# Performance work log

Hardware: AMD Instinct MI355X
Metric: run time of the kernel (lower is better)

Reference implementation:

```python
import jax, jax.numpy as jnp
import numpy as np
import math

B, S, D, H, HD, DC, FF, E, K = 4, 2048, 576, 9, 64, 64, 1536, 8, 2
EPS = 1e-6


def _rms(x):
    # RMSNorm with weight=ones (module instantiates a fresh RMSNorm in forward)
    return x / jnp.sqrt(jnp.mean(x * x, axis=-1, keepdims=True) + EPS)


def _expert(h, wa, wb, wc):
    return (jax.nn.gelu(h @ wa, approximate=False) * (h @ wc)) @ wb


def _forward(x, q_w, kv_w, o_w, gate_w, w1, w2, w3, sw1, sw2, sw3):
    # ---------------- MLA ----------------
    xn = _rms(x)
    q = (xn @ q_w).reshape(B, S, H, HD)
    kv = (xn @ kv_w).reshape(B, S, H, 2 * DC)
    k, v = kv[..., :DC], kv[..., DC:]
    # RoPE (complex-pair form) applied to q only, as in the source
    theta = 1.0 / (10000.0 ** (jnp.arange(0, HD, 2, dtype=jnp.float32) / HD))
    freqs = jnp.arange(S, dtype=jnp.float32)[:, None] * theta[None, :]  # [S, HD/2]
    cos = jnp.cos(freqs)[None, :, None, :]
    sin = jnp.sin(freqs)[None, :, None, :]
    qp = q.reshape(B, S, H, HD // 2, 2)
    qe, qo = qp[..., 0], qp[..., 1]
    q = jnp.stack([qe * cos - qo * sin, qe * sin + qo * cos], axis=-1).reshape(B, S, H, HD)
    # NOTE: source matmul attends head-vs-head per token: [B,S,H,HD] x [B,S,DC,H] -> [B,S,H,H]
    attn = jnp.einsum('bshd,bstd->bsht', q, k) / math.sqrt(HD)
    attn = jax.nn.softmax(attn, axis=-1)
    ao = jnp.einsum('bsht,bstd->bshd', attn, v)  # [B,S,H,DC]
    # faithful to torch: transpose(1,2).contiguous().view(B,S,D)
    ao = ao.transpose(0, 2, 1, 3).reshape(B, S, D)
    x = ao @ o_w + x
    # ---------------- MoE ----------------
    xn = _rms(x)
    gw = jax.nn.softmax(xn @ gate_w, axis=-1)  # [B,S,E]
    tw, ti = jax.lax.top_k(gw, K)
    tw = tw / jnp.sum(tw, axis=-1, keepdims=True)
    # combine weights per expert: zero for unselected experts (same math as masked loop)
    comb = jnp.sum(tw[..., None] * jax.nn.one_hot(ti, E, dtype=x.dtype), axis=-2)  # [B,S,E]
    h1 = jax.nn.gelu(jnp.einsum('bsd,edf->ebsf', xn, w1), approximate=False)
    h3 = jnp.einsum('bsd,edf->ebsf', xn, w3)
    eo = jnp.einsum('ebsf,efd->ebsd', h1 * h3, w2)  # [E,B,S,D]
    moe_out = jnp.einsum('ebsd,bse->bsd', eo, comb)
    shared = _expert(xn, sw1, sw2, sw3)
    return moe_out + shared + x


def setup_inputs() -> dict:
    key = jax.random.key(0)
    ks = jax.random.split(key, 11)
    s = 0.02
    return {
        'x': jax.random.normal(ks[0], (B, S, D), dtype=jnp.float32),
        'q_w': jax.random.normal(ks[1], (D, D), dtype=jnp.float32) * s,
        'kv_w': jax.random.normal(ks[2], (D, H * 2 * DC), dtype=jnp.float32) * s,
        'o_w': jax.random.normal(ks[3], (D, D), dtype=jnp.float32) * s,
        'gate_w': jax.random.normal(ks[4], (D, E), dtype=jnp.float32) * s,
        'w1': jax.random.normal(ks[5], (E, D, FF), dtype=jnp.float32) * s,
        'w2': jax.random.normal(ks[6], (E, FF, D), dtype=jnp.float32) * s,
        'w3': jax.random.normal(ks[7], (E, D, FF), dtype=jnp.float32) * s,
        'sw1': jax.random.normal(ks[8], (D, FF), dtype=jnp.float32) * s,
        'sw2': jax.random.normal(ks[9], (FF, D), dtype=jnp.float32) * s,
        'sw3': jax.random.normal(ks[10], (D, FF), dtype=jnp.float32) * s,
    }


def reference(x, q_w, kv_w, o_w, gate_w, w1, w2, w3, sw1, sw2, sw3):
    return _forward(x, q_w, kv_w, o_w, gate_w, w1, w2, w3, sw1, sw2, sw3)
```

## Files before the change

### kernel.cpp

```cpp
#include <hip/hip_runtime.h>
#include <math.h>

#define B_  4
#define S_  2048
#define D_  576
#define H_  9
#define HD_ 64
#define FF_ 1536
#define E_  8
#define TOK (B_*S_)
#define T1ROWS 17408

typedef unsigned int   u32x4  __attribute__((ext_vector_type(4)));
typedef unsigned short u16x8  __attribute__((ext_vector_type(8)));
typedef __bf16         bf16x8 __attribute__((ext_vector_type(8)));
typedef _Float16       f16x8  __attribute__((ext_vector_type(8)));
typedef float          f32x4  __attribute__((ext_vector_type(4)));

__device__ __forceinline__ float b2f(unsigned short u) {
    union { unsigned int i; float f; } v; v.i = ((unsigned int)u) << 16; return v.f;
}
__device__ __forceinline__ unsigned short f2b(float f) {
    unsigned int u = __builtin_bit_cast(unsigned int, f);
    unsigned int r = 0x7fffu + ((u >> 16) & 1u);
    return (unsigned short)((u + r) >> 16);
}

__global__ __launch_bounds__(256)
void rmsnorm_k(const float* __restrict__ x, unsigned short* __restrict__ xn) {
    int tok = blockIdx.x, tid = threadIdx.x;
    const float* xr = x + (size_t)tok * D_;
    float v0 = xr[tid];
    float v1 = xr[tid + 256];
    float v2 = (tid < D_ - 512) ? xr[tid + 512] : 0.f;
    float ss = v0*v0 + v1*v1 + v2*v2;
    #pragma unroll
    for (int d = 1; d < 64; d <<= 1) ss += __shfl_xor(ss, d, 64);
    __shared__ float red[4];
    if ((tid & 63) == 0) red[tid >> 6] = ss;
    __syncthreads();
    float tot = red[0] + red[1] + red[2] + red[3];
    float rms = rsqrtf(tot / (float)D_ + 1e-6f);
    unsigned short* orow = xn + (size_t)tok * D_;
    orow[tid]       = f2b(v0 * rms);
    orow[tid + 256] = f2b(v1 * rms);
    if (tid < D_ - 512) orow[tid + 512] = f2b(v2 * rms);
}

__global__ __launch_bounds__(256)
void rms32_k(const float* __restrict__ x, float* __restrict__ xn) {
    int tok = blockIdx.x, tid = threadIdx.x;
    const float* xr = x + (size_t)tok * D_;
    float v0 = xr[tid];
    float v1 = xr[tid + 256];
    float v2 = (tid < D_ - 512) ? xr[tid + 512] : 0.f;
    float ss = v0*v0 + v1*v1 + v2*v2;
    #pragma unroll
    for (int d = 1; d < 64; d <<= 1) ss += __shfl_xor(ss, d, 64);
    __shared__ float red[4];
    if ((tid & 63) == 0) red[tid >> 6] = ss;
    __syncthreads();
    float tot = red[0] + red[1] + red[2] + red[3];
    float rms = rsqrtf(tot / (float)D_ + 1e-6f);
    float* orow = xn + (size_t)tok * D_;
    orow[tid]       = v0 * rms;
    orow[tid + 256] = v1 * rms;
    if (tid < D_ - 512) orow[tid + 512] = v2 * rms;
}

__global__ __launch_bounds__(256)
void convw_k(const float* __restrict__ src, unsigned short* __restrict__ dst,
             int K, int N, long long sstr, long long dstr)
{
    __shared__ unsigned short t[64][72];
    int n0 = blockIdx.x * 64, k0 = blockIdx.y * 64;
    const float* s = src + (long long)blockIdx.z * sstr;
    unsigned short* d = dst + (long long)blockIdx.z * dstr;
    int tx = threadIdx.x & 63, ty = threadIdx.x >> 6;
    #pragma unroll
    for (int i = 0; i < 16; ++i) {
        int k = i * 4 + ty;
        t[k][tx] = f2b(s[(size_t)(k0 + k) * N + n0 + tx]);
    }
    __syncthreads();
    int r = threadIdx.x >> 3, c8 = (threadIdx.x & 7) * 8;
    #pragma unroll
    for (int it = 0; it < 2; ++it, r += 32) {
        u16x8 v;
        #pragma unroll
        for (int j = 0; j < 8; ++j) v[j] = t[c8 + j][r];
        *(u16x8*)&d[(size_t)(n0 + r) * K + k0 + c8] = v;
    }
}

template<int BN, int EPI>
__global__ __launch_bounds__(256)
void gemmS_k(const float* __restrict__ A, const float* __restrict__ Bm,
             float* __restrict__ Cout, const float* __restrict__ resid,
             int M, int N, int K, int ldb)
{
    constexpr int BM = 128, BK = 64, LDT = BK + 8;
    constexpr int WM = BM / 2, WN = BN / 2, MI = WM / 16, NJ = WN / 16;
    __shared__ alignas(16) _Float16 Ah[BM][LDT], Al[BM][LDT];
    __shared__ alignas(16) _Float16 Bh[BN][LDT], Bl[BN][LDT];
    const int tid  = threadIdx.x;
    const int bn0  = blockIdx.x * BN, bm0 = blockIdx.y * BM;
    const int lane = tid & 63, wave = tid >> 6;
    const int l    = lane & 15, quad = lane >> 4;
    const int wm   = wave >> 1, wn = wave & 1;

    f32x4 accH[MI][NJ], accL[MI][NJ];
    #pragma unroll
    for (int mi = 0; mi < MI; ++mi)
        #pragma unroll
        for (int nj = 0; nj < NJ; ++nj) {
            accH[mi][nj] = (f32x4){0.f, 0.f, 0.f, 0.f};
            accL[mi][nj] = (f32x4){0.f, 0.f, 0.f, 0.f};
        }

    const int nK = K / BK;
    for (int kc = 0; kc < nK; ++kc) {
        __syncthreads();
        #pragma unroll
        for (int i = 0; i < (BM * BK) / 2048; ++i) {
            int u = i * 256 + tid;
            int r = u >> 3, c8 = (u & 7) * 8;
            const float* ga = A + (size_t)(bm0 + r) * K + kc * BK + c8;
            f16x8 hh, ll;
            #pragma unroll
            for (int j = 0; j < 8; ++j) {
                float v = ga[j];
                _Float16 h = (_Float16)v;
                hh[j] = h;
                ll[j] = (_Float16)((v - (float)h) * 2048.0f);
            }
            *(f16x8*)&Ah[r][c8] = hh;
            *(f16x8*)&Al[r][c8] = ll;
        }
        #pragma unroll
        for (int i = 0; i < (BN * BK) / 2048; ++i) {
            int u = i * 256 + tid;
            int n = u % BN, k8 = (u / BN) * 8;
            const float* gB = Bm + (size_t)(kc * BK + k8) * ldb + bn0 + n;
            f16x8 hh, ll;
            #pragma unroll
            for (int j = 0; j < 8; ++j) {
                float v = gB[(size_t)j * ldb];
                _Float16 h = (_Float16)v;
                hh[j] = h;
                ll[j] = (_Float16)((v - (float)h) * 2048.0f);
            }
            *(f16x8*)&Bh[n][k8] = hh;
            *(f16x8*)&Bl[n][k8] = ll;
        }
        __syncthreads();
        #pragma unroll
        for (int ks = 0; ks < BK; ks += 32) {
            f16x8 ah[MI], al[MI], bh[NJ], bl[NJ];
            #pragma unroll
            for (int mi = 0; mi < MI; ++mi) {
                ah[mi] = *(const f16x8*)&Ah[wm * WM + mi * 16 + l][ks + quad * 8];
                al[mi] = *(const f16x8*)&Al[wm * WM + mi * 16 + l][ks + quad * 8];
            }
            #pragma unroll
            for (int nj = 0; nj < NJ; ++nj) {
                bh[nj] = *(const f16x8*)&Bh[wn * WN + nj * 16 + l][ks + quad * 8];
                bl[nj] = *(const f16x8*)&Bl[wn * WN + nj * 16 + l][ks + quad * 8];
            }
            #pragma unroll
            for (int mi = 0; mi < MI; ++mi)
                #pragma unroll
                for (int nj = 0; nj < NJ; ++nj) {
                    accH[mi][nj] = __builtin_amdgcn_mfma_f32_16x16x32_f16(
                        ah[mi], bh[nj], accH[mi][nj], 0, 0, 0);
                    accL[mi][nj] = __builtin_amdgcn_mfma_f32_16x16x32_f16(
                        ah[mi], bl[nj], accL[mi][nj], 0, 0, 0);
                    accL[mi][nj] = __builtin_amdgcn_mfma_f32_16x16x32_f16(
                        al[mi], bh[nj], accL[mi][nj], 0, 0, 0);
                }
        }
    }
    #pragma unroll
    for (int mi = 0; mi < MI; ++mi)
        #pragma unroll
        for (int nj = 0; nj < NJ; ++nj)
            #pragma unroll
            for (int r = 0; r < 4; ++r) {
                int row = bm0 + wm * WM + mi * 16 + quad * 4 + r;
                int col = bn0 + wn * WN + nj * 16 + l;
                float v = accH[mi][nj][r] + accL[mi][nj][r] * (1.0f / 2048.0f);
                size_t idx = (size_t)row * N + col;
                if constexpr (EPI == 0) Cout[idx] = v;
                else                    Cout[idx] = v + resid[idx];
            }
}

template<int ROUTED>
__global__ __launch_bounds__(256, 2)
void gemm13_k(const unsigned short* __restrict__ A,
              const unsigned short* __restrict__ B1,
              const unsigned short* __restrict__ B3,
              unsigned short* __restrict__ T1o,
              const int* __restrict__ eidx,
              const int* __restrict__ counts,
              const int* __restrict__ offs,
              int M, int N, long long bstr)
{
    constexpr int BM = 128, BN = 128, BK = 64, LDT = BK + 8;
    constexpr int MI = 4, NJ = 4;
    __shared__ alignas(16) unsigned short As[BM][LDT];
    __shared__ alignas(16) unsigned short Bs1[BN][LDT];
    __shared__ alignas(16) unsigned short Bs3[BN][LDT];
    __shared__ int rowbuf[BM];
    const int tid  = threadIdx.x;
    const int bn0  = blockIdx.x * BN, bm0 = blockIdx.y * BM;
    const int lane = tid & 63, wave = tid >> 6;
    const int l    = lane & 15, quad = lane >> 4;
    const int wm   = wave >> 1, wn = wave & 1;
    const int rs   = tid >> 3, c8 = (tid & 7) * 8;

    int cnt = M, crow0 = 0;
    if constexpr (ROUTED) {
        int e = blockIdx.z;
        cnt = counts[e];
        if (bm0 >= cnt) return;
        crow0 = offs[e];
        B1 += (long long)e * bstr;
        B3 += (long long)e * bstr;
        if (tid < BM) {
            int rr = bm0 + tid;
            rowbuf[tid] = (rr < cnt) ? eidx[e * TOK + rr] : 0;
        }
        __syncthreads();
    }

    f32x4 acc1[MI][NJ], acc3[MI][NJ];
    #pragma unroll
    for (int mi = 0; mi < MI; ++mi)
        #pragma unroll
        for (int nj = 0; nj < NJ; ++nj) {
            acc1[mi][nj] = (f32x4){0.f, 0.f, 0.f, 0.f};
            acc3[mi][nj] = (f32x4){0.f, 0.f, 0.f, 0.f};
        }

    const int nK = D_ / BK;
    u32x4 ra[4], rb1[4], rb3[4];
    #pragma unroll
    for (int i = 0; i < 4; ++i) {
        int r = i * 32 + rs;
        int arow = ROUTED ? rowbuf[r] : (bm0 + r);
        ra[i]  = *(const u32x4*)(A  + (size_t)arow * D_ + c8);
        rb1[i] = *(const u32x4*)(B1 + (size_t)(bn0 + r) * D_ + c8);
        rb3[i] = *(const u32x4*)(B3 + (size_t)(bn0 + r) * D_ + c8);
    }
    for (int kc = 0; kc < nK; ++kc) {
        __syncthreads();
        #pragma unroll
        for (int i = 0; i < 4; ++i) {
            int r = i * 32 + rs;
            *(u32x4*)&As[r][c8]  = ra[i];
            *(u32x4*)&Bs1[r][c8] = rb1[i];
            *(u32x4*)&Bs3[r][c8] = rb3[i];
        }
        __syncthreads();
        if (kc + 1 < nK) {
            int ko = (kc + 1) * BK;
            #pragma unroll
            for (int i = 0; i < 4; ++i) {
                int r = i * 32 + rs;
                int arow = ROUTED ? rowbuf[r] : (bm0 + r);
                ra[i]  = *(const u32x4*)(A  + (size_t)arow * D_ + ko + c8);
                rb1[i] = *(const u32x4*)(B1 + (size_t)(bn0 + r) * D_ + ko + c8);
                rb3[i] = *(const u32x4*)(B3 + (size_t)(bn0 + r) * D_ + ko + c8);
            }
        }
        #pragma unroll
        for (int ks = 0; ks < BK; ks += 32) {
            bf16x8 af[MI], b1f[NJ], b3f[NJ];
            #pragma unroll
            for (int mi = 0; mi < MI; ++mi)
                af[mi] = __builtin_bit_cast(bf16x8,
                    *(const u32x4*)&As[wm * 64 + mi * 16 + l][ks + quad * 8]);
            #pragma unroll
            for (int nj = 0; nj < NJ; ++nj) {
                b1f[nj] = __builtin_bit_cast(bf16x8,
                    *(const u32x4*)&Bs1[wn * 64 + nj * 16 + l][ks + quad * 8]);
                b3f[nj] = __builtin_bit_cast(bf16x8,
                    *(const u32x4*)&Bs3[wn * 64 + nj * 16 + l][ks + quad * 8]);
            }
            #pragma unroll
            for (int mi = 0; mi < MI; ++mi)
                #pragma unroll
                for (int nj = 0; nj < NJ; ++nj) {
                    acc1[mi][nj] = __builtin_amdgcn_mfma_f32_16x16x32_bf16(
                        af[mi], b1f[nj], acc1[mi][nj], 0, 0, 0);
                    acc3[mi][nj] = __builtin_amdgcn_mfma_f32_16x16x32_bf16(
                        af[mi], b3f[nj], acc3[mi][nj], 0, 0, 0);
                }
        }
    }
    #pragma unroll
    for (int mi = 0; mi < MI; ++mi)
        #pragma unroll
        for (int nj = 0; nj < NJ; ++nj)
            #pragma unroll
            for (int r = 0; r < 4; ++r) {
                int lrow = bm0 + wm * 64 + mi * 16 + quad * 4 + r;
                int col  = bn0 + wn * 64 + nj * 16 + l;
                float hv = b2f(f2b(acc1[mi][nj][r]));
                float g  = 0.5f * hv * (1.0f + erff(hv * 0.70710678118654752f));
                T1o[(size_t)(crow0 + lrow) * N + col] = f2b(g * acc3[mi][nj][r]);
            }
}

template<int BN, int EPI, int ROUTED, int WB>
__global__ __launch_bounds__(256)
void gemm_k(const unsigned short* __restrict__ A,
            const void* __restrict__ Bm,
            void* __restrict__ Cout,
            const void* __restrict__ resid,
            const float* __restrict__ wgt,
            const int* __restrict__ eidx,
            const int* __restrict__ counts,
            const int* __restrict__ offs,
            int M, int N, int K, int ldb, long long bstr)
{
    constexpr int BM = 128, BK = 64, LDT = BK + 8;
    constexpr int WM = BM / 2, WN = BN / 2, MI = WM / 16, NJ = WN / 16;
    constexpr int AIT = (BM * BK) / 2048, BIT = (BN * BK) / 2048;
    __shared__ alignas(16) unsigned short As[BM][LDT];
    __shared__ alignas(16) unsigned short Bs[BN][LDT];
    __shared__ int rowbuf[BM];
    const int tid  = threadIdx.x;
    const int bn0  = blockIdx.x * BN, bm0 = blockIdx.y * BM;
    const int lane = tid & 63, wave = tid >> 6;
    const int l    = lane & 15, quad = lane >> 4;
    const int wm   = wave >> 1, wn = wave & 1;

    int cnt = M, crow0 = 0, ebase = 0;
    long long boff = 0;
    if constexpr (ROUTED) {
        int e = blockIdx.z;
        cnt = counts[e];
        if (bm0 >= cnt) return;
        crow0 = offs[e];
        ebase = e * TOK;
        boff  = (long long)e * bstr;
        if (tid < BM) {
            int rr = bm0 + tid;
            rowbuf[tid] = (rr < cnt) ? eidx[ebase + rr] : 0;
        }
        __syncthreads();
    }

    f32x4 acc[MI][NJ];
    #pragma unroll
    for (int mi = 0; mi < MI; ++mi)
        #pragma unroll
        for (int nj = 0; nj < NJ; ++nj) acc[mi][nj] = (f32x4){0.f, 0.f, 0.f, 0.f};

    const int nK = K / BK;
    u32x4 pa[AIT], pb[BIT];
    if constexpr (WB == 1) {
        const unsigned short* Bt = (const unsigned short*)Bm + boff;
        #pragma unroll
        for (int i = 0; i < AIT; ++i) {
            int r = i * 32 + (tid >> 3), c8 = (tid & 7) * 8;
            int arow;
            if constexpr (ROUTED && EPI != 5) arow = rowbuf[r];
            else if constexpr (ROUTED)        arow = crow0 + bm0 + r;
            else                              arow = bm0 + r;
            pa[i] = *(const u32x4*)(A + (size_t)arow * K + c8);
        }
        #pragma unroll
        for (int i = 0; i < BIT; ++i) {
            int n = i * 32 + (tid >> 3), c8 = (tid & 7) * 8;
            pb[i] = *(const u32x4*)(Bt + (size_t)(bn0 + n) * ldb + c8);
        }
    }
    for (int kc = 0; kc < nK; ++kc) {
        __syncthreads();
        if constexpr (WB == 1) {
            #pragma unroll
            for (int i = 0; i < AIT; ++i) {
                int r = i * 32 + (tid >> 3), c8 = (tid & 7) * 8;
                *(u32x4*)&As[r][c8] = pa[i];
            }
            #pragma unroll
            for (int i = 0; i < BIT; ++i) {
                int n = i * 32 + (tid >> 3), c8 = (tid & 7) * 8;
                *(u32x4*)&Bs[n][c8] = pb[i];
            }
        } else {
            #pragma unroll
            for (int i = 0; i < AIT; ++i) {
                int u = i * 256 + tid;
                int r = u >> 3, c8 = (u & 7) * 8;
                int arow;
                if constexpr (ROUTED && EPI != 5) arow = rowbuf[r];
                else if constexpr (ROUTED)        arow = crow0 + bm0 + r;
                else                              arow = bm0 + r;
                *(u32x4*)&As[r][c8] =
                    *(const u32x4*)(A + (size_t)arow * K + kc * BK + c8);
            }
            const float* Bf = (const float*)Bm + boff;
            #pragma unroll
            for (int i = 0; i < BIT; ++i) {
                int u = i * 256 + tid;
                int n = u % BN, k8 = (u / BN) * 8;
                const float* gB = Bf + (size_t)(kc * BK + k8) * ldb + bn0 + n;
                u16x8 tmp;
                #pragma unroll
                for (int j = 0; j < 8; ++j) tmp[j] = f2b(gB[(size_t)j * ldb]);
                *(u16x8*)&Bs[n][k8] = tmp;
            }
        }
        __syncthreads();
        if constexpr (WB == 1) {
            if (kc + 1 < nK) {
                int ko = (kc + 1) * BK;
                const unsigned short* Bt = (const unsigned short*)Bm + boff;
                #pragma unroll
                for (int i = 0; i < AIT; ++i) {
                    int r = i * 32 + (tid >> 3), c8 = (tid & 7) * 8;
                    int arow;
                    if constexpr (ROUTED && EPI != 5) arow = rowbuf[r];
                    else if constexpr (ROUTED)        arow = crow0 + bm0 + r;
                    else                              arow = bm0 + r;
                    pa[i] = *(const u32x4*)(A + (size_t)arow * K + ko + c8);
                }
                #pragma unroll
                for (int i = 0; i < BIT; ++i) {
                    int n = i * 32 + (tid >> 3), c8 = (tid & 7) * 8;
                    pb[i] = *(const u32x4*)(Bt + (size_t)(bn0 + n) * ldb + ko + c8);
                }
            }
        }
        #pragma unroll
        for (int ks = 0; ks < BK; ks += 32) {
            bf16x8 af[MI], bfr[NJ];
            #pragma unroll
            for (int mi = 0; mi < MI; ++mi)
                af[mi] = __builtin_bit_cast(bf16x8,
                    *(const u32x4*)&As[wm * WM + mi * 16 + l][ks + quad * 8]);
            #pragma unroll
            for (int nj = 0; nj < NJ; ++nj)
                bfr[nj] = __builtin_bit_cast(bf16x8,
                    *(const u32x4*)&Bs[wn * WN + nj * 16 + l][ks + quad * 8]);
            #pragma unroll
            for (int mi = 0; mi < MI; ++mi)
                #pragma unroll
                for (int nj = 0; nj < NJ; ++nj)
                    acc[mi][nj] = __builtin_amdgcn_mfma_f32_16x16x32_bf16(
                        af[mi], bfr[nj], acc[mi][nj], 0, 0, 0);
        }
    }
    #pragma unroll
    for (int mi = 0; mi < MI; ++mi)
        #pragma unroll
        for (int nj = 0; nj < NJ; ++nj)
            #pragma unroll
            for (int r = 0; r < 4; ++r) {
                int lrow = bm0 + wm * WM + mi * 16 + quad * 4 + r;
                int col  = bn0 + wn * WN + nj * 16 + l;
                float v = acc[mi][nj][r];
                if constexpr (EPI == 0) {
                    ((unsigned short*)Cout)[(size_t)(crow0 + lrow) * N + col] = f2b(v);
                } else if constexpr (EPI == 3) {
                    size_t ix = (size_t)(crow0 + lrow) * N + col;
                    float hv = b2f(((const unsigned short*)resid)[ix]);
                    float g = 0.5f * hv * (1.0f + erff(hv * 0.70710678118654752f));
                    ((unsigned short*)Cout)[ix] = f2b(g * v);
                } else if constexpr (EPI == 4) {
                    ((float*)Cout)[(size_t)lrow * N + col] += v;
                } else {
                    if (lrow < cnt) {
                        int   tok = rowbuf[lrow - bm0];
                        float sc  = wgt[ebase + lrow];
                        atomicAdd(&((float*)Cout)[(size_t)tok * N + col], sc * v);
                    }
                }
            }
}

__global__ __launch_bounds__(256)
void attn32_k(const float* __restrict__ q,
              const float* __restrict__ kv,
              float* __restrict__ ao,
              int pos0)
{
    int pl   = blockIdx.x * 4 + (threadIdx.x >> 6);
    int lane = threadIdx.x & 63;
    int pos  = pos0 + pl;
    int b = pos >> 11, s = pos & 2047;

    const float* qp  = q  + (size_t)pl * 576;
    const float* kvp = kv + (size_t)pl * 1152;

    int i = lane >> 1;
    float theta = powf(10000.f, -(float)i * (1.0f / 32.0f));
    float sn, cs;
    sincosf((float)s * theta, &sn, &cs);

    float qr[H_], kr[H_], vr[H_];
    #pragma unroll
    for (int h = 0; h < H_; ++h) {
        float qv = qp[h * 64 + lane];
        float qo = __shfl_xor(qv, 1, 64);
        qr[h] = (lane & 1) ? (qo * sn + qv * cs) : (qv * cs - qo * sn);
        kr[h] = kvp[h * 128 + lane];
        vr[h] = kvp[h * 128 + 64 + lane];
    }

    #pragma unroll
    for (int h = 0; h < H_; ++h) {
        float sc[H_];
        #pragma unroll
        for (int t = 0; t < H_; ++t) {
            float p = qr[h] * kr[t];
            #pragma unroll
            for (int d = 1; d < 64; d <<= 1) p += __shfl_xor(p, d, 64);
            sc[t] = p * 0.125f;
        }
        float mx = sc[0];
        #pragma unroll
        for (int t = 1; t < H_; ++t) mx = fmaxf(mx, sc[t]);
        float ssum = 0.f;
        #pragma unroll
        for (int t = 0; t < H_; ++t) { sc[t] = __expf(sc[t] - mx); ssum += sc[t]; }
        float inv = 1.0f / ssum;
        float ov = 0.f;
        #pragma unroll
        for (int t = 0; t < H_; ++t) ov += sc[t] * vr[t];
        ao[((size_t)(b * H_ + h) * S_ + s) * 64 + lane] = ov * inv;
    }
}

__global__ __launch_bounds__(256)
void gate1_k(const float* __restrict__ x2,
             const float* __restrict__ gw,
             float* __restrict__ tw,
             int*   __restrict__ tsel)
{
    int tok  = blockIdx.x * 4 + (threadIdx.x >> 6);
    int lane = threadIdx.x & 63;
    float acc[8];
    #pragma unroll
    for (int e = 0; e < 8; ++e) acc[e] = 0.f;
    float ss = 0.f;
    for (int d = lane; d < D_; d += 64) {
        float xv = x2[(size_t)tok * D_ + d];
        ss += xv * xv;
        const float* wr = gw + (size_t)d * 8;
        #pragma unroll
        for (int e = 0; e < 8; ++e) acc[e] += xv * wr[e];
    }
    #pragma unroll
    for (int d = 1; d < 64; d <<= 1) ss += __shfl_xor(ss, d, 64);
    #pragma unroll
    for (int e = 0; e < 8; ++e)
        #pragma unroll
        for (int d = 1; d < 64; d <<= 1) acc[e] += __shfl_xor(acc[e], d, 64);
    if (lane == 0) {
        float rms = rsqrtf(ss / (float)D_ + 1e-6f);
        #pragma unroll
        for (int e = 0; e < 8; ++e) acc[e] *= rms;
        float mx = acc[0];
        #pragma unroll
        for (int e = 1; e < 8; ++e) mx = fmaxf(mx, acc[e]);
        float g[8], ssum = 0.f;
        #pragma unroll
        for (int e = 0; e < 8; ++e) { g[e] = __expf(acc[e] - mx); ssum += g[e]; }
        #pragma unroll
        for (int e = 0; e < 8; ++e) g[e] /= ssum;
        int i1 = 0;
        #pragma unroll
        for (int e = 1; e < 8; ++e) if (g[e] > g[i1]) i1 = e;
        int i2 = -1;
        #pragma unroll
        for (int e = 0; e < 8; ++e)
            if (e != i1 && (i2 < 0 || g[e] > g[i2])) i2 = e;
        float s2 = g[i1] + g[i2];
        tw[(size_t)tok * 2 + 0] = g[i1] / s2;
        tw[(size_t)tok * 2 + 1] = g[i2] / s2;
        tsel[tok] = i1 | (i2 << 8);
    }
}

__global__ __launch_bounds__(256)
void gate2_k(const int*   __restrict__ tsel,
             const float* __restrict__ tw,
             float* __restrict__ wgt,
             int*   __restrict__ eidx,
             int*   __restrict__ counts)
{
    int e    = blockIdx.x;
    int tid  = threadIdx.x;
    int lane = tid & 63, wv = tid >> 6;
    __shared__ int wtot[4];
    int base = 0;
    for (int t0 = 0; t0 < TOK; t0 += 256) {
        int tok = t0 + tid;
        int s = tsel[tok];
        int hit = 0; float w = 0.f;
        if ((s & 255) == e)      { hit = 1; w = tw[(size_t)tok * 2 + 0]; }
        else if ((s >> 8) == e)  { hit = 1; w = tw[(size_t)tok * 2 + 1]; }
        unsigned long long m = __ballot(hit);
        int pre = __popcll(m & ((1ull << lane) - 1ull));
        if (lane == 0) wtot[wv] = __popcll(m);
        __syncthreads();
        int off = base;
        for (int q = 0; q < wv; ++q) off += wtot[q];
        if (hit) {
            int p = off + pre;
            eidx[e * TOK + p] = tok;
            wgt [e * TOK + p] = w;
        }
        base += wtot[0] + wtot[1] + wtot[2] + wtot[3];
        __syncthreads();
    }
    if (tid == 0) counts[e] = base;
}

__global__ void offs_k(const int* __restrict__ counts, int* __restrict__ offs) {
    if (threadIdx.x == 0) {
        int run = 0;
        for (int e = 0; e < 8; ++e) {
            offs[e] = run;
            run += ((counts[e] + 127) >> 7) << 7;
        }
    }
}

extern "C" void kernel_launch(void* const* d_in, const int* in_sizes, int n_in,
                              void* d_out, int out_size, void* d_ws, size_t ws_size,
                              hipStream_t stream)
{
    const float* x      = (const float*)d_in[0];
    const float* q_w    = (const float*)d_in[1];
    const float* kv_w   = (const float*)d_in[2];
    const float* o_w    = (const float*)d_in[3];
    const float* gate_w = (const float*)d_in[4];
    const float* w1     = (const float*)d_in[5];
    const float* w2     = (const float*)d_in[6];
    const float* w3     = (const float*)d_in[7];
    const float* sw1    = (const float*)d_in[8];
    const float* sw2    = (const float*)d_in[9];
    const float* sw3    = (const float*)d_in[10];
    float* out = (float*)d_out;

    const size_t XN = (size_t)TOK * D_ * 2;
    char* ws = (char*)d_ws;
    unsigned short* xn16 = (unsigned short*)ws;
    float*          ao32 = (float*)(ws + XN);

    int TC = 64;
    if      (3*XN + 8*XN    <= ws_size) TC = 1;
    else if (3*XN + 8*XN/2  <= ws_size) TC = 2;
    else if (3*XN + 8*XN/4  <= ws_size) TC = 4;
    else if (3*XN + 8*XN/8  <= ws_size) TC = 8;
    else if (3*XN + 8*XN/16 <= ws_size) TC = 16;
    else if (3*XN + 8*XN/32 <= ws_size) TC = 32;
    const int CT = TOK / TC;
    float* xn32c = (float*)(ws + 3*XN);
    float* qc    = xn32c + (size_t)CT * D_;
    float* kvc   = qc    + (size_t)CT * D_;

    int*   counts = (int*)(ws + XN);
    int*   offs   = counts + 16;
    float* wgt    = (float*)(ws + XN + 256);
    int*   eidx   = (int*)  (ws + XN + 256 + (size_t)8 * TOK * 4);
    float* tw     = (float*)(ws + XN + 256 + (size_t)8 * TOK * 8);
    int*   tsel   = (int*)  (ws + XN + 256 + (size_t)8 * TOK * 8 + (size_t)TOK * 8);
    const size_t fixedG = XN + 256 + (size_t)8 * TOK * 8 + (size_t)TOK * 12;

    const size_t WELEM = (size_t)D_ * FF_;
    const size_t WSZ   = 27 * WELEM * 2;
    const size_t t1sz  = (size_t)T1ROWS * FF_ * 2;

    bool conv; int FC;
    if      (fixedG + WSZ + t1sz   <= ws_size) { conv = true;  FC = 1; }
    else if (fixedG + WSZ + t1sz/2 <= ws_size) { conv = true;  FC = 2; }
    else if (fixedG + WSZ + t1sz/4 <= ws_size) { conv = true;  FC = 4; }
    else if (fixedG + t1sz         <= ws_size) { conv = false; FC = 1; }
    else if (fixedG + t1sz/2       <= ws_size) { conv = false; FC = 2; }
    else                                       { conv = false; FC = 4; }
    const int FFc = FF_ / FC;

    unsigned short* wt1  = (unsigned short*)(ws + fixedG);
    unsigned short* wt3  = wt1 + 8 * WELEM;
    unsigned short* wt2  = wt3 + 8 * WELEM;
    unsigned short* swt1 = wt2 + 8 * WELEM;
    unsigned short* swt3 = swt1 + WELEM;
    unsigned short* swt2 = swt3 + WELEM;
    unsigned short* t1   = (unsigned short*)(ws + fixedG + (conv ? WSZ : 0));

    for (int t = 0; t < TC; ++t) {
        const float* xc = x + (size_t)t * CT * D_;
        rms32_k<<<CT, 256, 0, stream>>>(xc, xn32c);
        gemmS_k<64, 0><<<dim3(D_ / 64, CT / 128), 256, 0, stream>>>(
            xn32c, q_w, qc, nullptr, CT, D_, D_, D_);
        gemmS_k<64, 0><<<dim3(1152 / 64, CT / 128), 256, 0, stream>>>(
            xn32c, kv_w, kvc, nullptr, CT, 1152, D_, 1152);
        attn32_k<<<CT / 4, 256, 0, stream>>>(qc, kvc, ao32, t * CT);
    }
    gemmS_k<64, 1><<<dim3(D_ / 64, TOK / 128), 256, 0, stream>>>(
        ao32, o_w, out, x, TOK, D_, D_, D_);
    rmsnorm_k<<<TOK, 256, 0, stream>>>(out, xn16);
    gate1_k<<<TOK / 4, 256, 0, stream>>>(out, gate_w, tw, tsel);
    gate2_k<<<E_, 256, 0, stream>>>(tsel, tw, wgt, eidx, counts);
    offs_k<<<1, 64, 0, stream>>>(counts, offs);
    if (conv) {
        convw_k<<<dim3(FF_/64, D_/64, 8), 256, 0, stream>>>(
            w1, wt1, D_, FF_, (long long)D_ * FF_, (long long)FF_ * D_);
        convw_k<<<dim3(FF_/64, D_/64, 8), 256, 0, stream>>>(
            w3, wt3, D_, FF_, (long long)D_ * FF_, (long long)FF_ * D_);
        convw_k<<<dim3(D_/64, FF_/64, 8), 256, 0, stream>>>(
            w2, wt2, FF_, D_, (long long)FF_ * D_, (long long)D_ * FF_);
        convw_k<<<dim3(FF_/64, D_/64, 1), 256, 0, stream>>>(
            sw1, swt1, D_, FF_, 0, 0);
        convw_k<<<dim3(FF_/64, D_/64, 1), 256, 0, stream>>>(
            sw3, swt3, D_, FF_, 0, 0);
        convw_k<<<dim3(D_/64, FF_/64, 1), 256, 0, stream>>>(
            sw2, swt2, FF_, D_, 0, 0);
    }
    for (int c = 0; c < FC; ++c) {
        if (conv) {
            gemm13_k<1><<<dim3(FFc / 128, TOK / 128, E_), 256, 0, stream>>>(
                xn16, wt1 + (size_t)c * FFc * D_, wt3 + (size_t)c * FFc * D_,
                t1, eidx, counts, offs, TOK, FFc, (long long)FF_ * D_);
            gemm_k<64, 5, 1, 1><<<dim3(D_ / 64, TOK / 128, E_), 256, 0, stream>>>(
                t1, wt2 + (size_t)c * FFc, out, nullptr, wgt, eidx, counts, offs,
                TOK, D_, FFc, FF_, (long long)D_ * FF_);
            gemm13_k<0><<<dim3(FFc / 128, TOK / 128), 256, 0, stream>>>(
                xn16, swt1 + (size_t)c * FFc * D_, swt3 + (size_t)c * FFc * D_,
                t1, nullptr, nullptr, nullptr, TOK, FFc, 0);
            gemm_k<64, 4, 0, 1><<<dim3(D_ / 64, TOK / 128), 256, 0, stream>>>(
                t1, swt2 + (size_t)c * FFc, out, nullptr, nullptr, nullptr, nullptr, nullptr,
                TOK, D_, FFc, FF_, 0);
        } else {
            const float* w1c = w1 + (size_t)c * FFc;
            const float* w3c = w3 + (size_t)c * FFc;
            const float* w2c = w2 + (size_t)c * FFc * D_;
            gemm_k<128, 0, 1, 0><<<dim3(FFc / 128, TOK / 128, E_), 256, 0, stream>>>(
                xn16, w1c, t1, nullptr, wgt, eidx, counts, offs,
                TOK, FFc, D_, FF_, (long long)D_ * FF_);
            gemm_k<128, 3, 1, 0><<<dim3(FFc / 128, TOK / 128, E_), 256, 0, stream>>>(
                xn16, w3c, t1, t1, wgt, eidx, counts, offs,
                TOK, FFc, D_, FF_, (long long)D_ * FF_);
            gemm_k<64, 5, 1, 0><<<dim3(D_ / 64, TOK / 128, E_), 256, 0, stream>>>(
                t1, w2c, out, nullptr, wgt, eidx, counts, offs,
                TOK, D_, FFc, D_, (long long)FF_ * D_);
            gemm_k<128, 0, 0, 0><<<dim3(FFc / 128, TOK / 128), 256, 0, stream>>>(
                xn16, sw1 + (size_t)c * FFc, t1, nullptr, nullptr, nullptr, nullptr, nullptr,
                TOK, FFc, D_, FF_, 0);
            gemm_k<128, 3, 0, 0><<<dim3(FFc / 128, TOK / 128), 256, 0, stream>>>(
                xn16, sw3 + (size_t)c * FFc, t1, t1, nullptr, nullptr, nullptr, nullptr,
                TOK, FFc, D_, FF_, 0);
            gemm_k<64, 4, 0, 0><<<dim3(D_ / 64, TOK / 128), 256, 0, stream>>>(
                t1, sw2 + (size_t)c * FFc * D_, out, nullptr, nullptr, nullptr, nullptr, nullptr,
                TOK, D_, FFc, D_, 0);
        }
    }
}
```

Measured before the change: 710.0 us.

## Pre-split attention weights into fp16 hi/lo once and widen MoE down-proj tiles

Adds a conversion kernel that transposes q_w, kv_w and o_w once into fp16 high/low split buffers. The split-precision attention GEMMs then load B tiles with contiguous vector copies instead of strided fp32 loads and per-element conversion inside every block. Separately, the MoE and shared down-projection GEMMs switch from BN=64 to BN=192 tiles, so fewer blocks re-read the A operand. The costs are extra workspace, which may force more token chunks when workspace is tight, three small extra launches, and higher register and LDS pressure in the wider tiles.

```diff
diff --git a/kernel.cpp b/kernel.cpp
--- a/kernel.cpp
+++ b/kernel.cpp
@@ -93,9 +93,38 @@
     }
 }
 
-template<int BN, int EPI>
+__global__ __launch_bounds__(256)
+void convS_k(const float* __restrict__ src,
+             _Float16* __restrict__ dh, _Float16* __restrict__ dl,
+             int K, int N)
+{
+    __shared__ _Float16 th[64][72], tl[64][72];
+    int n0 = blockIdx.x * 64, k0 = blockIdx.y * 64;
+    int tx = threadIdx.x & 63, ty = threadIdx.x >> 6;
+    #pragma unroll
+    for (int i = 0; i < 16; ++i) {
+        int k = i * 4 + ty;
+        float v = src[(size_t)(k0 + k) * N + n0 + tx];
+        _Float16 h = (_Float16)v;
+        th[k][tx] = h;
+        tl[k][tx] = (_Float16)((v - (float)h) * 2048.0f);
+    }
+    __syncthreads();
+    int r = threadIdx.x >> 3, c8 = (threadIdx.x & 7) * 8;
+    #pragma unroll
+    for (int it = 0; it < 2; ++it, r += 32) {
+        f16x8 vh, vl;
+        #pragma unroll
+        for (int j = 0; j < 8; ++j) { vh[j] = th[c8 + j][r]; vl[j] = tl[c8 + j][r]; }
+        *(f16x8*)&dh[(size_t)(n0 + r) * K + k0 + c8] = vh;
+        *(f16x8*)&dl[(size_t)(n0 + r) * K + k0 + c8] = vl;
+    }
+}
+
+template<int BN, int EPI, int WB>
 __global__ __launch_bounds__(256)
 void gemmS_k(const float* __restrict__ A, const float* __restrict__ Bm,
+             const _Float16* __restrict__ Bhp, const _Float16* __restrict__ Blp,
              float* __restrict__ Cout, const float* __restrict__ resid,
              int M, int N, int K, int ldb)
 {
@@ -137,21 +166,33 @@
             *(f16x8*)&Ah[r][c8] = hh;
             *(f16x8*)&Al[r][c8] = ll;
         }
-        #pragma unroll
-        for (int i = 0; i < (BN * BK) / 2048; ++i) {
-            int u = i * 256 + tid;
-            int n = u % BN, k8 = (u / BN) * 8;
-            const float* gB = Bm + (size_t)(kc * BK + k8) * ldb + bn0 + n;
-            f16x8 hh, ll;
-            #pragma unroll
-            for (int j = 0; j < 8; ++j) {
-                float v = gB[(size_t)j * ldb];
-                _Float16 h = (_Float16)v;
-                hh[j] = h;
-                ll[j] = (_Float16)((v - (float)h) * 2048.0f);
-            }
-            *(f16x8*)&Bh[n][k8] = hh;
-            *(f16x8*)&Bl[n][k8] = ll;
+        if constexpr (WB == 1) {
+            #pragma unroll
+            for (int i = 0; i < (BN * BK) / 2048; ++i) {
+                int u = i * 256 + tid;
+                int n = u >> 3, c8 = (u & 7) * 8;
+                *(f16x8*)&Bh[n][c8] =
+                    *(const f16x8*)(Bhp + (size_t)(bn0 + n) * K + kc * BK + c8);
+                *(f16x8*)&Bl[n][c8] =
+                    *(const f16x8*)(Blp + (size_t)(bn0 + n) * K + kc * BK + c8);
+            }
+        } else {
+            #pragma unroll
+            for (int i = 0; i < (BN * BK) / 2048; ++i) {
+                int u = i * 256 + tid;
+                int n = u % BN, k8 = (u / BN) * 8;
+                const float* gB = Bm + (size_t)(kc * BK + k8) * ldb + bn0 + n;
+                f16x8 hh, ll;
+                #pragma unroll
+                for (int j = 0; j < 8; ++j) {
+                    float v = gB[(size_t)j * ldb];
+                    _Float16 h = (_Float16)v;
+                    hh[j] = h;
+                    ll[j] = (_Float16)((v - (float)h) * 2048.0f);
+                }
+                *(f16x8*)&Bh[n][k8] = hh;
+                *(f16x8*)&Bl[n][k8] = ll;
+            }
         }
         __syncthreads();
         #pragma unroll
@@ -654,15 +695,31 @@
     unsigned short* xn16 = (unsigned short*)ws;
     float*          ao32 = (float*)(ws + XN);
 
-    int TC = 64;
-    if      (3*XN + 8*XN    <= ws_size) TC = 1;
-    else if (3*XN + 8*XN/2  <= ws_size) TC = 2;
-    else if (3*XN + 8*XN/4  <= ws_size) TC = 4;
-    else if (3*XN + 8*XN/8  <= ws_size) TC = 8;
-    else if (3*XN + 8*XN/16 <= ws_size) TC = 16;
-    else if (3*XN + 8*XN/32 <= ws_size) TC = 32;
+    const size_t QE = (size_t)D_ * D_, KVE = (size_t)1152 * D_;
+    const size_t SW = (2 * QE + KVE) * 2 * 2;
+    _Float16* qwh  = (_Float16*)(ws + 3 * XN);
+    _Float16* qwl  = qwh  + QE;
+    _Float16* kvwh = qwl  + QE;
+    _Float16* kvwl = kvwh + KVE;
+    _Float16* owh  = kvwl + KVE;
+    _Float16* owl  = owh  + QE;
+
+    bool convA = true;
+    int TC = -1;
+    for (int pass = 0; pass < 2; ++pass) {
+        size_t base = 3 * XN + (convA ? SW : 0);
+        if      (base + 8*XN    <= ws_size) { TC = 1; break; }
+        else if (base + 8*XN/2  <= ws_size) { TC = 2; break; }
+        else if (base + 8*XN/4  <= ws_size) { TC = 4; break; }
+        else if (base + 8*XN/8  <= ws_size) { TC = 8; break; }
+        else if (base + 8*XN/16 <= ws_size) { TC = 16; break; }
+        else if (base + 8*XN/32 <= ws_size) { TC = 32; break; }
+        else if (base + 8*XN/64 <= ws_size) { TC = 64; break; }
+        convA = false;
+    }
+    if (TC < 0) { convA = false; TC = 64; }
     const int CT = TOK / TC;
-    float* xn32c = (float*)(ws + 3*XN);
+    float* xn32c = (float*)(ws + 3*XN + (convA ? SW : 0));
     float* qc    = xn32c + (size_t)CT * D_;
     float* kvc   = qc    + (size_t)CT * D_;
 
@@ -695,17 +752,33 @@
     unsigned short* swt2 = swt3 + WELEM;
     unsigned short* t1   = (unsigned short*)(ws + fixedG + (conv ? WSZ : 0));
 
+    if (convA) {
+        convS_k<<<dim3(D_/64,  D_/64), 256, 0, stream>>>(q_w,  qwh,  qwl,  D_, D_);
+        convS_k<<<dim3(1152/64, D_/64), 256, 0, stream>>>(kv_w, kvwh, kvwl, D_, 1152);
+        convS_k<<<dim3(D_/64,  D_/64), 256, 0, stream>>>(o_w,  owh,  owl,  D_, D_);
+    }
     for (int t = 0; t < TC; ++t) {
         const float* xc = x + (size_t)t * CT * D_;
         rms32_k<<<CT, 256, 0, stream>>>(xc, xn32c);
-        gemmS_k<64, 0><<<dim3(D_ / 64, CT / 128), 256, 0, stream>>>(
-            xn32c, q_w, qc, nullptr, CT, D_, D_, D_);
-        gemmS_k<64, 0><<<dim3(1152 / 64, CT / 128), 256, 0, stream>>>(
-            xn32c, kv_w, kvc, nullptr, CT, 1152, D_, 1152);
+        if (convA) {
+            gemmS_k<64, 0, 1><<<dim3(D_ / 64, CT / 128), 256, 0, stream>>>(
+                xn32c, nullptr, qwh, qwl, qc, nullptr, CT, D_, D_, D_);
+            gemmS_k<64, 0, 1><<<dim3(1152 / 64, CT / 128), 256, 0, stream>>>(
+                xn32c, nullptr, kvwh, kvwl, kvc, nullptr, CT, 1152, D_, D_);
+        } else {
+            gemmS_k<64, 0, 0><<<dim3(D_ / 64, CT / 128), 256, 0, stream>>>(
+                xn32c, q_w, nullptr, nullptr, qc, nullptr, CT, D_, D_, D_);
+            gemmS_k<64, 0, 0><<<dim3(1152 / 64, CT / 128), 256, 0, stream>>>(
+                xn32c, kv_w, nullptr, nullptr, kvc, nullptr, CT, 1152, D_, 1152);
+        }
         attn32_k<<<CT / 4, 256, 0, stream>>>(qc, kvc, ao32, t * CT);
     }
-    gemmS_k<64, 1><<<dim3(D_ / 64, TOK / 128), 256, 0, stream>>>(
-        ao32, o_w, out, x, TOK, D_, D_, D_);
+    if (convA)
+        gemmS_k<64, 1, 1><<<dim3(D_ / 64, TOK / 128), 256, 0, stream>>>(
+            ao32, nullptr, owh, owl, out, x, TOK, D_, D_, D_);
+    else
+        gemmS_k<64, 1, 0><<<dim3(D_ / 64, TOK / 128), 256, 0, stream>>>(
+            ao32, o_w, nullptr, nullptr, out, x, TOK, D_, D_, D_);
     rmsnorm_k<<<TOK, 256, 0, stream>>>(out, xn16);
     gate1_k<<<TOK / 4, 256, 0, stream>>>(out, gate_w, tw, tsel);
     gate2_k<<<E_, 256, 0, stream>>>(tsel, tw, wgt, eidx, counts);
@@ -729,13 +802,13 @@
             gemm13_k<1><<<dim3(FFc / 128, TOK / 128, E_), 256, 0, stream>>>(
                 xn16, wt1 + (size_t)c * FFc * D_, wt3 + (size_t)c * FFc * D_,
                 t1, eidx, counts, offs, TOK, FFc, (long long)FF_ * D_);
-            gemm_k<64, 5, 1, 1><<<dim3(D_ / 64, TOK / 128, E_), 256, 0, stream>>>(
+            gemm_k<192, 5, 1, 1><<<dim3(D_ / 192, TOK / 128, E_), 256, 0, stream>>>(
                 t1, wt2 + (size_t)c * FFc, out, nullptr, wgt, eidx, counts, offs,
                 TOK, D_, FFc, FF_, (long long)D_ * FF_);
             gemm13_k<0><<<dim3(FFc / 128, TOK / 128), 256, 0, stream>>>(
                 xn16, swt1 + (size_t)c * FFc * D_, swt3 + (size_t)c * FFc * D_,
                 t1, nullptr, nullptr, nullptr, TOK, FFc, 0);
-            gemm_k<64, 4, 0, 1><<<dim3(D_ / 64, TOK / 128), 256, 0, stream>>>(
+            gemm_k<192, 4, 0, 1><<<dim3(D_ / 192, TOK / 128), 256, 0, stream>>>(
                 t1, swt2 + (size_t)c * FFc, out, nullptr, nullptr, nullptr, nullptr, nullptr,
                 TOK, D_, FFc, FF_, 0);
         } else {
```

After: 704.1 us. No clear change (-0.8%).
